# Kernel optimization log

Measured on AMD Instinct MI355X. Metric: run time of the kernel, lower is better.

## Reference

```python
import math
import jax, jax.numpy as jnp
import numpy as np
from jax import lax

D = 384; NHEAD = 12; NLAYERS = 4; H = 128; WIN = (128, 24); NS = (1, 10); B = 256; CONV_C = 128

def _interleave(s, c):
    # [s0,c0,s1,c1,...] along last dim (matches 0::2=sin, 1::2=cos)
    return jnp.stack([s, c], axis=-1).reshape(s.shape[:-1] + (s.shape[-1] * 2,))

def _pos_encoding():
    d3 = D // 3
    div = jnp.exp(jnp.arange(0, d3, 2, dtype=jnp.float32) * (-math.log(10000.0) / d3))
    coord = jnp.arange(H, dtype=jnp.float32) - H // 2
    pe1d = _interleave(jnp.sin(coord[:, None] * div), jnp.cos(coord[:, None] * div))  # (H, d3)
    pe_y = jnp.broadcast_to(pe1d[:, None, :], (H, H, d3))
    pe_x = jnp.broadcast_to(pe1d[None, :, :], (H, H, d3))
    ws = jnp.array(WIN, dtype=jnp.float32)
    pe_w = _interleave(jnp.sin(ws[:, None] * div), jnp.cos(ws[:, None] * div))  # (2, d3)
    pe_yx = jnp.concatenate([pe_y, pe_x], axis=-1)  # (H, H, 2*d3)
    pe = jnp.concatenate([
        jnp.broadcast_to(pe_yx[:, :, None, :], (H, H, len(WIN), 2 * d3)),
        jnp.broadcast_to(pe_w[None, None, :, :], (H, H, len(WIN), d3))], axis=-1)
    return pe  # (H, H, 2, D)

def _windows(img3, pos, ws):
    # img3: (B,3,H,W); pos: (n,2) int. Crop [y1:y2, x1:x2] then zero-pad bottom/right to ws x ws.
    hw = ws // 2
    y = jnp.clip(pos[:, 0], 0, H - 1); x = jnp.clip(pos[:, 1], 0, H - 1)
    y1 = jnp.maximum(0, y - hw); y2 = jnp.minimum(H, y + hw)
    x1 = jnp.maximum(0, x - hw); x2 = jnp.minimum(H, x + hw)
    r = jnp.arange(ws)
    rows = y1[:, None] + r; cols = x1[:, None] + r  # (n, ws)
    mask = (rows < y2[:, None])[:, :, None] & (cols < x2[:, None])[:, None, :]  # (n, ws, ws)
    win = img3[:, :, jnp.clip(rows, 0, H - 1)[:, :, None], jnp.clip(cols, 0, H - 1)[:, None, :]]  # (B,3,n,ws,ws)
    win = jnp.where(mask[None, None], win, 0.0)
    return jnp.transpose(win, (0, 2, 1, 3, 4))  # (B, n, 3, ws, ws)

def _layer_norm(x, g, b):
    m = x.mean(-1, keepdims=True)
    v = ((x - m) ** 2).mean(-1, keepdims=True)
    return (x - m) / jnp.sqrt(v + 1e-5) * g + b

def _encoder_layer(x, Wqkv, bqkv, Wo, bo, g1, b1, g2, b2, W1, bf1, W2, bf2):
    Bsz, S, _ = x.shape
    dh = D // NHEAD
    qkv = x @ Wqkv.T + bqkv
    q, k, v = jnp.split(qkv, 3, axis=-1)
    heads = lambda t: t.reshape(Bsz, S, NHEAD, dh).transpose(0, 2, 1, 3)
    q, k, v = heads(q), heads(k), heads(v)
    att = jax.nn.softmax(jnp.einsum('bhqd,bhkd->bhqk', q, k) / math.sqrt(dh), axis=-1)
    o = jnp.einsum('bhqk,bhkd->bhqd', att, v).transpose(0, 2, 1, 3).reshape(Bsz, S, D)
    x = _layer_norm(x + o @ Wo.T + bo, g1, b1)
    ff = jax.nn.relu(x @ W1.T + bf1) @ W2.T + bf2
    return _layer_norm(x + ff, g2, b2)

def _normalize(v):
    return v / jnp.maximum(jnp.linalg.norm(v, axis=1, keepdims=True), 1e-12)

def _forward(pos0, pos1, rgb_image, conv_w, conv_b, ext_w, ext_b, proj_w, proj_b,
             Wqkv, bqkv, Wo, bo, ln1g, ln1b, ln2g, ln2b, Wff1, bff1, Wff2, bff2,
             rw1, rb1, rw2, rb2, uw1, ub1, uw2, ub2):
    Bsz = rgb_image.shape[0]
    img3 = rgb_image[:, :3]
    win0 = _windows(img3, pos0, WIN[0]).reshape(Bsz * NS[0], 3, WIN[0], WIN[0])
    win1 = _windows(img3, pos1, WIN[1])  # (B, 10, 3, 24, 24)
    h = lax.conv_general_dilated(win0, conv_w, (4, 4), 'SAME')
    h = jax.nn.relu(h + conv_b[None, :, None, None])
    f0 = (h.mean((2, 3)) @ ext_w.T + ext_b).reshape(Bsz, NS[0], D)
    f1 = win1.reshape(Bsz, NS[1], -1) @ proj_w.T + proj_b  # (B,10,D)
    feats = jnp.concatenate([f0, f1], axis=1)  # (B, 11, D)
    pe = _pos_encoding()
    pp = jnp.concatenate([
        jnp.concatenate([pos0, jnp.zeros((NS[0], 1), pos0.dtype)], axis=1),
        jnp.concatenate([pos1, jnp.ones((NS[1], 1), pos1.dtype)], axis=1)], axis=0)  # (11, 3)
    pf = pe[pp[:, 0], pp[:, 1], pp[:, 2]]  # (11, D)
    x = feats + pf[None]
    for i in range(NLAYERS):
        x = _encoder_layer(x, Wqkv[i], bqkv[i], Wo[i], bo[i], ln1g[i], ln1b[i],
                           ln2g[i], ln2b[i], Wff1[i], bff1[i], Wff2[i], bff2[i])
    m = x.mean(axis=1)
    r = jax.nn.relu(m @ rw1.T + rb1) @ rw2.T + rb2
    r1, r2 = r[:, :3], r[:, 3:]
    r2 = r2 - jnp.sum(r1 * r2, axis=1, keepdims=True) * r1
    r3 = jnp.cross(r1, r2)
    R = jnp.concatenate([_normalize(r1), _normalize(r2), _normalize(r3)], axis=1)
    uv = jax.nn.sigmoid(jax.nn.relu(m @ uw1.T + ub1) @ uw2.T + ub2)
    return (uv, R)

def setup_inputs():
    key = jax.random.key(0)
    ks = iter(jax.random.split(key, 40))
    w = lambda *s: jax.random.normal(next(ks), s, jnp.float32) * 0.02
    return dict(
        rgb_image=jax.random.uniform(next(ks), (B, 4, H, H), jnp.float32),
        pos0=jax.random.randint(next(ks), (NS[0], 2), 0, H).astype(jnp.int32),
        pos1=jax.random.randint(next(ks), (NS[1], 2), 0, H).astype(jnp.int32),
        conv_w=w(CONV_C, 3, 7, 7), conv_b=jnp.zeros((CONV_C,), jnp.float32),
        ext_w=w(D, CONV_C), ext_b=jnp.zeros((D,), jnp.float32),
        proj_w=w(D, WIN[1] * WIN[1] * 3), proj_b=jnp.zeros((D,), jnp.float32),
        Wqkv=w(NLAYERS, 3 * D, D), bqkv=jnp.zeros((NLAYERS, 3 * D), jnp.float32),
        Wo=w(NLAYERS, D, D), bo=jnp.zeros((NLAYERS, D), jnp.float32),
        ln1g=jnp.ones((NLAYERS, D), jnp.float32), ln1b=jnp.zeros((NLAYERS, D), jnp.float32),
        ln2g=jnp.ones((NLAYERS, D), jnp.float32), ln2b=jnp.zeros((NLAYERS, D), jnp.float32),
        Wff1=w(NLAYERS, 2048, D), bff1=jnp.zeros((NLAYERS, 2048), jnp.float32),
        Wff2=w(NLAYERS, D, 2048), bff2=jnp.zeros((NLAYERS, D), jnp.float32),
        rw1=w(D, D), rb1=jnp.zeros((D,), jnp.float32),
        rw2=w(6, D), rb2=jnp.zeros((6,), jnp.float32),
        uw1=w(D, D), ub1=jnp.zeros((D,), jnp.float32),
        uw2=w(2, D), ub2=jnp.zeros((2,), jnp.float32),
    )

def reference(rgb_image, pos0, pos1, conv_w, conv_b, ext_w, ext_b, proj_w, proj_b,
              Wqkv, bqkv, Wo, bo, ln1g, ln1b, ln2g, ln2b, Wff1, bff1, Wff2, bff2,
              rw1, rb1, rw2, rb2, uw1, ub1, uw2, ub2):
    return _forward(pos0, pos1, rgb_image, conv_w, conv_b, ext_w, ext_b, proj_w, proj_b,
                    Wqkv, bqkv, Wo, bo, ln1g, ln1b, ln2g, ln2b, Wff1, bff1, Wff2, bff2,
                    rw1, rb1, rw2, rb2, uw1, ub1, uw2, ub2)
```

## Files before the change

kernel.cpp:

```cpp
#include <hip/hip_runtime.h>
#include <hip/hip_bf16.h>

#define B_ 256
#define S_ 11
#define D_ 384
#define NHEAD_ 12

typedef const float* bfp;
typedef __attribute__((ext_vector_type(8))) __bf16 bf16x8;
typedef __attribute__((ext_vector_type(4))) float f32x4;

__device__ __forceinline__ bf16x8 ld8_b64(const __bf16* p) {
    union { unsigned long long q[2]; bf16x8 v; } u;
    u.q[0] = *reinterpret_cast<const unsigned long long*>(p);
    u.q[1] = *reinterpret_cast<const unsigned long long*>(p + 4);
    return u.v;
}

__device__ __forceinline__ void gl16(const __bf16* g, __bf16* l) {
    __builtin_amdgcn_global_load_lds(
        (const __attribute__((address_space(1))) void*)g,
        (__attribute__((address_space(3))) void*)l, 16, 0, 0);
}

__global__ void f2b_k(const float* __restrict__ s, __bf16* __restrict__ d, int n4)
{
    int i = blockIdx.x * 256 + threadIdx.x;
    if (i >= n4) return;
    float4 v = reinterpret_cast<const float4*>(s)[i];
    union { __bf16 h[4]; unsigned long long u; } p;
    p.h[0] = (__bf16)v.x; p.h[1] = (__bf16)v.y;
    p.h[2] = (__bf16)v.z; p.h[3] = (__bf16)v.w;
    reinterpret_cast<unsigned long long*>(d)[i] = p.u;
}

__global__ void prep_wpad_k(bfp __restrict__ cw, __bf16* __restrict__ wpad)
{
    int e = blockIdx.x * 256 + threadIdx.x;
    if (e >= 3072) return;
    int r = e >> 5, g = e & 31;
    if (g >= 24) return;
    union { __bf16 h[8]; uint4 u; } w;
    #pragma unroll
    for (int kx = 0; kx < 8; ++kx) {
        float v = 0.f;
        if (g < 21 && kx < 7) v = cw[(size_t)r * 147 + g * 7 + kx];
        w.h[kx] = (__bf16)v;
    }
    *reinterpret_cast<uint4*>(&wpad[(size_t)r * 192 + g * 8]) = w.u;
}

__global__ __launch_bounds__(256) void gemm_bb_k(
    const __bf16* __restrict__ A, const __bf16* __restrict__ W,
    const float* __restrict__ bias, const float* __restrict__ resid,
    void* __restrict__ C_, int M, int N, int K, int mode, int outBf16, int kChunk)
{
    __shared__ __align__(16) __bf16 AsF[4096];
    __shared__ __align__(16) __bf16 WsF[4096];
    const int tid = threadIdx.x;
    const int bm = blockIdx.y * 64, bn = blockIdx.x * 64;
    const int z = blockIdx.z;
    int kStart = 0, kEnd = K;
    if (kChunk) { kStart = z * kChunk; kEnd = min(K, kStart + kChunk); }
    const int lane = tid & 63, wv = tid >> 6;
    const int wr = (wv >> 1) * 32, wc = (wv & 1) * 32;
    const int lr = lane & 15, lk = lane >> 4;
    const int c1 = tid + 256;
    const int r0 = tid >> 3, j0 = (tid & 7) ^ (r0 & 7);
    const int r1 = c1 >> 3,  j1 = (c1 & 7) ^ (r1 & 7);
    __bf16* ldsA0 = AsF + (wv << 9);
    __bf16* ldsA1 = AsF + 2048 + (wv << 9);
    __bf16* ldsW0 = WsF + (wv << 9);
    __bf16* ldsW1 = WsF + 2048 + (wv << 9);
    f32x4 acc[2][2] = {};
    for (int k0 = kStart; k0 < kEnd; k0 += 64) {
        const __bf16* ga0 = A + (size_t)(bm + r0) * K + k0 + j0 * 8;
        const __bf16* ga1 = A + (size_t)(bm + r1) * K + k0 + j1 * 8;
        const __bf16* gw0 = W + (size_t)(bn + r0) * K + k0 + j0 * 8;
        const __bf16* gw1 = W + (size_t)(bn + r1) * K + k0 + j1 * 8;
        __syncthreads();
        gl16(ga0, ldsA0);
        gl16(ga1, ldsA1);
        gl16(gw0, ldsW0);
        gl16(gw1, ldsW1);
        __syncthreads();
        #pragma unroll
        for (int s = 0; s < 2; ++s) {
            int j = s * 4 + lk;
            int ra0 = wr + lr,  ra1 = wr + 16 + lr;
            int rw0 = wc + lr,  rw1 = wc + 16 + lr;
            bf16x8 a0 = *reinterpret_cast<const bf16x8*>(&AsF[ra0 * 64 + ((j ^ (ra0 & 7)) << 3)]);
            bf16x8 a1 = *reinterpret_cast<const bf16x8*>(&AsF[ra1 * 64 + ((j ^ (ra1 & 7)) << 3)]);
            bf16x8 w0 = *reinterpret_cast<const bf16x8*>(&WsF[rw0 * 64 + ((j ^ (rw0 & 7)) << 3)]);
            bf16x8 w1 = *reinterpret_cast<const bf16x8*>(&WsF[rw1 * 64 + ((j ^ (rw1 & 7)) << 3)]);
            acc[0][0] = __builtin_amdgcn_mfma_f32_16x16x32_bf16(a0, w0, acc[0][0], 0, 0, 0);
            acc[0][1] = __builtin_amdgcn_mfma_f32_16x16x32_bf16(a0, w1, acc[0][1], 0, 0, 0);
            acc[1][0] = __builtin_amdgcn_mfma_f32_16x16x32_bf16(a1, w0, acc[1][0], 0, 0, 0);
            acc[1][1] = __builtin_amdgcn_mfma_f32_16x16x32_bf16(a1, w1, acc[1][1], 0, 0, 0);
        }
    }
    if (kChunk) {
        float* Cp = (float*)C_ + (size_t)z * M * N;
        #pragma unroll
        for (int m = 0; m < 2; ++m)
            #pragma unroll
            for (int n = 0; n < 2; ++n) {
                int col = bn + wc + n * 16 + lr;
                #pragma unroll
                for (int i = 0; i < 4; ++i) {
                    int row = bm + wr + m * 16 + lk * 4 + i;
                    Cp[(size_t)row * N + col] = acc[m][n][i];
                }
            }
    } else {
        #pragma unroll
        for (int m = 0; m < 2; ++m)
            #pragma unroll
            for (int n = 0; n < 2; ++n) {
                int col = bn + wc + n * 16 + lr;
                float bcol = bias[col];
                #pragma unroll
                for (int i = 0; i < 4; ++i) {
                    int row = bm + wr + m * 16 + lk * 4 + i;
                    float v = acc[m][n][i] + bcol;
                    if (mode == 1) v = fmaxf(v, 0.f);
                    if (mode == 2) v += resid[(size_t)row * N + col];
                    if (outBf16) ((__bf16*)C_)[(size_t)row * N + col] = (__bf16)v;
                    else         ((float*)C_)[(size_t)row * N + col] = v;
                }
            }
    }
}

__global__ __launch_bounds__(256) void convgemm_k(
    bfp __restrict__ img, const __bf16* __restrict__ wpad, bfp __restrict__ cb,
    const int* __restrict__ pos0, float* __restrict__ f0pre)
{
    __shared__ __align__(16) __bf16 Wlds[64][200];
    __shared__ __align__(16) __bf16 P[3][12][136];
    const int tid = threadIdx.x;
    const int blk = blockIdx.x;
    const int b = blk >> 3;
    const int bn = ((blk >> 2) & 1) * 64;
    const int mtg = blk & 3;
    int y = min(max(pos0[0], 0), 127), x = min(max(pos0[1], 0), 127);
    int y1 = max(0, y - 64), y2 = min(128, y + 64);
    int x1 = max(0, x - 64), x2 = min(128, x + 64);
    const int lane = tid & 63, wv = tid >> 6;
    const int wr = (wv >> 1) * 32, wc = (wv & 1) * 32;
    const int lr = lane & 15, lk = lane >> 4;
    const int oyl = wr >> 5;
    const int ox0 = lr, ox1 = 16 + lr;

    for (int e = tid; e < 1536; e += 256) {
        int r = e / 24, g = e - r * 24;
        uint4 q = *reinterpret_cast<const uint4*>(&wpad[(size_t)(bn + r) * 192 + g * 8]);
        *reinterpret_cast<uint4*>(&Wlds[r][g * 8]) = q;
    }

    float s0 = 0.f, s1 = 0.f;
    const float bc0 = cb[bn + wc + lr];
    const float bc1 = cb[bn + wc + 16 + lr];

    for (int t = 0; t < 4; ++t) {
        int mt = mtg * 4 + t;
        __syncthreads();
        for (int e = tid; e < 2448; e += 256) {
            int c = e / 816, rem = e - c * 816;
            int r2 = rem / 68, ip2 = (rem - r2 * 68) * 2;
            int rl = mt * 8 - 1 + r2;
            bool rok = (rl >= 0) && ((y1 + rl) < y2);
            const float* row = img + ((size_t)(b * 4 + c) * 128 + y1 + rl) * 128 + x1;
            int cl0 = ip2 - 1, cl1 = ip2;
            float v0 = 0.f, v1 = 0.f;
            if (rok && cl0 >= 0 && (x1 + cl0) < x2) v0 = row[cl0];
            if (rok && (x1 + cl1) < x2)             v1 = row[cl1];
            union { __bf16 h[2]; unsigned int u; } p;
            p.h[0] = (__bf16)v0; p.h[1] = (__bf16)v1;
            *reinterpret_cast<unsigned int*>(&P[c][r2][ip2]) = p.u;
        }
        __syncthreads();
        f32x4 acc[2][2] = {};
        #pragma unroll
        for (int kk = 0; kk < 6; ++kk) {
            int g = kk * 4 + lk;
            int c = g / 7, ky = g - c * 7;
            if (g >= 21) { c = 0; ky = 0; }
            const __bf16* prow = &P[c][oyl * 4 + ky][0];
            bf16x8 a0 = ld8_b64(prow + ox0 * 4);
            bf16x8 a1 = ld8_b64(prow + ox1 * 4);
            bf16x8 w0 = *reinterpret_cast<const bf16x8*>(&Wlds[wc + lr][g * 8]);
            bf16x8 w1 = *reinterpret_cast<const bf16x8*>(&Wlds[wc + 16 + lr][g * 8]);
            acc[0][0] = __builtin_amdgcn_mfma_f32_16x16x32_bf16(a0, w0, acc[0][0], 0, 0, 0);
            acc[0][1] = __builtin_amdgcn_mfma_f32_16x16x32_bf16(a0, w1, acc[0][1], 0, 0, 0);
            acc[1][0] = __builtin_amdgcn_mfma_f32_16x16x32_bf16(a1, w0, acc[1][0], 0, 0, 0);
            acc[1][1] = __builtin_amdgcn_mfma_f32_16x16x32_bf16(a1, w1, acc[1][1], 0, 0, 0);
        }
        #pragma unroll
        for (int m = 0; m < 2; ++m)
            #pragma unroll
            for (int i = 0; i < 4; ++i) {
                s0 += fmaxf(acc[m][0][i] + bc0, 0.f);
                s1 += fmaxf(acc[m][1][i] + bc1, 0.f);
            }
    }
    s0 += __shfl_xor(s0, 16); s0 += __shfl_xor(s0, 32);
    s1 += __shfl_xor(s1, 16); s1 += __shfl_xor(s1, 32);
    if (lk == 0) {
        atomicAdd(&f0pre[b * 128 + bn + wc + lr],      s0 * (1.f / 1024.f));
        atomicAdd(&f0pre[b * 128 + bn + wc + 16 + lr], s1 * (1.f / 1024.f));
    }
}

#define BM 64
#define BN 64
#define BK 16
__global__ __launch_bounds__(256) void gemm_k(
    const float* __restrict__ A, bfp __restrict__ W,
    bfp __restrict__ bias, const float* __restrict__ resid,
    float* __restrict__ C, int M, int N, int K, int mode)
{
    __shared__ __align__(16) float As[BK][BM + 4];
    __shared__ __align__(16) float Ws[BK][BN + 4];
    const int tx = threadIdx.x & 15, ty = threadIdx.x >> 4;
    const int bm = blockIdx.y * BM, bn = blockIdx.x * BN;
    float acc[4][4] = {};
    for (int k0 = 0; k0 < K; k0 += BK) {
        for (int e = threadIdx.x; e < BM * BK; e += 256) {
            int r = e >> 4, kk = e & 15;
            As[kk][r] = A[(size_t)(bm + r) * K + k0 + kk];
        }
        for (int e = threadIdx.x; e < BN * BK; e += 256) {
            int c = e >> 4, kk = e & 15;
            Ws[kk][c] = W[(size_t)(bn + c) * K + k0 + kk];
        }
        __syncthreads();
        #pragma unroll
        for (int kk = 0; kk < BK; ++kk) {
            float4 av = *reinterpret_cast<const float4*>(&As[kk][ty * 4]);
            float4 wv = *reinterpret_cast<const float4*>(&Ws[kk][tx * 4]);
            float a[4] = {av.x, av.y, av.z, av.w};
            float w[4] = {wv.x, wv.y, wv.z, wv.w};
            #pragma unroll
            for (int i = 0; i < 4; ++i)
                #pragma unroll
                for (int j = 0; j < 4; ++j) acc[i][j] += a[i] * w[j];
        }
        __syncthreads();
    }
    #pragma unroll
    for (int i = 0; i < 4; ++i) {
        int row = bm + ty * 4 + i;
        #pragma unroll
        for (int j = 0; j < 4; ++j) {
            int col = bn + tx * 4 + j;
            float v = acc[i][j] + bias[col];
            if (mode == 1) v = fmaxf(v, 0.f);
            if (mode == 2) v += resid[(size_t)row * N + col];
            C[(size_t)row * N + col] = v;
        }
    }
}

__global__ void f0_k(const float* __restrict__ f0pre, bfp __restrict__ ew,
                     bfp __restrict__ eb, float* __restrict__ fbuf0)
{
    int b = blockIdx.x, d = threadIdx.x;
    __shared__ float pre[128];
    if (d < 128) pre[d] = f0pre[b * 128 + d];
    __syncthreads();
    float acc = eb[d];
    for (int co = 0; co < 128; ++co) acc += pre[co] * ew[d * 128 + co];
    fbuf0[b * 384 + d] = acc;
}

__global__ void win1_k(bfp __restrict__ img, const int* __restrict__ pos1,
                       __bf16* __restrict__ w1)
{
    int i = blockIdx.x * 256 + threadIdx.x;
    if (i >= B_ * 10 * 1728) return;
    int cc = i % 24, r = (i / 24) % 24, c = (i / 576) % 3, s = (i / 1728) % 10, b = i / 17280;
    int y = min(max(pos1[s * 2], 0), 127), x = min(max(pos1[s * 2 + 1], 0), 127);
    int y1 = max(0, y - 12), y2 = min(128, y + 12);
    int x1 = max(0, x - 12), x2 = min(128, x + 12);
    float v = 0.f;
    if ((y1 + r) < y2 && (x1 + cc) < x2)
        v = img[((size_t)(b * 4 + c) * 128 + (y1 + r)) * 128 + (x1 + cc)];
    w1[i] = (__bf16)v;
}

__global__ void pf_k(const int* __restrict__ pos0, const int* __restrict__ pos1,
                     float* __restrict__ pf)
{
    int d = threadIdx.x;
    const float c1 = -logf(10000.f) / 128.f;
    for (int s = 0; s < 11; ++s) {
        int py, px, pw;
        if (s == 0) { py = pos0[0]; px = pos0[1]; pw = 0; }
        else { py = pos1[(s - 1) * 2]; px = pos1[(s - 1) * 2 + 1]; pw = 1; }
        float coordv; int dd = d;
        if (d < 128) coordv = (float)(py - 64);
        else if (d < 256) { coordv = (float)(px - 64); dd = d - 128; }
        else { coordv = (pw == 0) ? 128.f : 24.f; dd = d - 256; }
        int i = dd >> 1;
        float div = expf((float)(2 * i) * c1);
        float ang = coordv * div;
        pf[s * 384 + d] = (dd & 1) ? cosf(ang) : sinf(ang);
    }
}

__global__ void assemble_k(const float* __restrict__ f0, const float* __restrict__ f1,
                           const float* __restrict__ pf, float* __restrict__ x,
                           __bf16* __restrict__ xb)
{
    int i = blockIdx.x * 256 + threadIdx.x;
    if (i >= B_ * S_ * D_) return;
    int d = i % 384, s = (i / 384) % 11, b = i / (384 * 11);
    float f = (s == 0) ? f0[b * 384 + d] : f1[((size_t)(b * 10) + (s - 1)) * 384 + d];
    float v = f + pf[s * 384 + d];
    x[i] = v;
    xb[i] = (__bf16)v;
}

__global__ __launch_bounds__(128) void attn_k(const float* __restrict__ qkv,
                                              __bf16* __restrict__ obuf)
{
    int b = blockIdx.x / NHEAD_, h = blockIdx.x % NHEAD_;
    __shared__ float q[11][32], k[11][32], v[11][32], att[11][12];
    for (int e = threadIdx.x; e < 352; e += 128) {
        int s = e >> 5, d = e & 31;
        size_t base = (size_t)(b * 11 + s) * 1152 + h * 32 + d;
        q[s][d] = qkv[base];
        k[s][d] = qkv[base + 384];
        v[s][d] = qkv[base + 768];
    }
    __syncthreads();
    if (threadIdx.x < 121) {
        int i = threadIdx.x / 11, j = threadIdx.x % 11;
        float s = 0.f;
        #pragma unroll
        for (int d = 0; d < 32; ++d) s += q[i][d] * k[j][d];
        att[i][j] = s * 0.17677669529663687f;
    }
    __syncthreads();
    if (threadIdx.x < 11) {
        int i = threadIdx.x;
        float mx = att[i][0];
        for (int j = 1; j < 11; ++j) mx = fmaxf(mx, att[i][j]);
        float e_[11], sum = 0.f;
        for (int j = 0; j < 11; ++j) { e_[j] = expf(att[i][j] - mx); sum += e_[j]; }
        float inv = 1.f / sum;
        for (int j = 0; j < 11; ++j) att[i][j] = e_[j] * inv;
    }
    __syncthreads();
    for (int e = threadIdx.x; e < 352; e += 128) {
        int i = e >> 5, d = e & 31;
        float s = 0.f;
        #pragma unroll
        for (int j = 0; j < 11; ++j) s += att[i][j] * v[j][d];
        obuf[(size_t)(b * 11 + i) * 384 + h * 32 + d] = (__bf16)s;
    }
}

__global__ __launch_bounds__(512) void ln_k(const float* __restrict__ parts, int nparts,
                                            const float* __restrict__ resid,
                                            const float* __restrict__ bias,
                                            bfp g, bfp be, float* __restrict__ xo,
                                            __bf16* __restrict__ xb)
{
    int row = blockIdx.x * 8 + (threadIdx.x >> 6);
    int lane = threadIdx.x & 63;
    const size_t MN = (size_t)2816 * 384;
    float v[6];
    float s = 0.f, sq = 0.f;
    #pragma unroll
    for (int j = 0; j < 6; ++j) {
        int d = lane + 64 * j;
        size_t off = (size_t)row * 384 + d;
        float t = resid[off] + bias[d];
        for (int z = 0; z < nparts; ++z) t += parts[z * MN + off];
        v[j] = t; s += t; sq += t * t;
    }
    #pragma unroll
    for (int o = 32; o >= 1; o >>= 1) { s += __shfl_xor(s, o); sq += __shfl_xor(sq, o); }
    float mean = s * (1.f / 384.f);
    float var = sq * (1.f / 384.f) - mean * mean;
    float inv = rsqrtf(var + 1e-5f);
    float* xr = xo + (size_t)row * 384;
    __bf16* xbr = xb + (size_t)row * 384;
    #pragma unroll
    for (int j = 0; j < 6; ++j) {
        int d = lane + 64 * j;
        float o = (v[j] - mean) * inv * g[d] + be[d];
        xr[d] = o;
        xbr[d] = (__bf16)o;
    }
}

__global__ void mean_k(const float* __restrict__ x, float* __restrict__ m)
{
    int b = blockIdx.x, d = threadIdx.x;
    float s = 0.f;
    for (int si = 0; si < 11; ++si) s += x[((size_t)b * 11 + si) * 384 + d];
    m[b * 384 + d] = s * (1.f / 11.f);
}

__global__ __launch_bounds__(64) void head_k(const float* __restrict__ h1,
    const float* __restrict__ h2, bfp __restrict__ rw2, bfp __restrict__ rb2,
    bfp __restrict__ uw2, bfp __restrict__ ub2, float* __restrict__ out)
{
    int b = blockIdx.x, lane = threadIdx.x;
    float acc[8] = {};
    for (int d = lane; d < 384; d += 64) {
        float a1 = h1[b * 384 + d], a2 = h2[b * 384 + d];
        #pragma unroll
        for (int o = 0; o < 6; ++o) acc[o] += a1 * rw2[o * 384 + d];
        acc[6] += a2 * uw2[d];
        acc[7] += a2 * uw2[384 + d];
    }
    #pragma unroll
    for (int o = 0; o < 8; ++o)
        #pragma unroll
        for (int off = 32; off >= 1; off >>= 1) acc[o] += __shfl_xor(acc[o], off);
    if (lane == 0) {
        float r[6];
        for (int o = 0; o < 6; ++o) r[o] = acc[o] + rb2[o];
        float u0 = acc[6] + ub2[0], u1 = acc[7] + ub2[1];
        float dot12 = r[0] * r[3] + r[1] * r[4] + r[2] * r[5];
        float q2x = r[3] - dot12 * r[0], q2y = r[4] - dot12 * r[1], q2z = r[5] - dot12 * r[2];
        float q3x = r[1] * q2z - r[2] * q2y;
        float q3y = r[2] * q2x - r[0] * q2z;
        float q3z = r[0] * q2y - r[1] * q2x;
        float n1 = fmaxf(sqrtf(r[0]*r[0] + r[1]*r[1] + r[2]*r[2]), 1e-12f);
        float n2 = fmaxf(sqrtf(q2x*q2x + q2y*q2y + q2z*q2z), 1e-12f);
        float n3 = fmaxf(sqrtf(q3x*q3x + q3y*q3y + q3z*q3z), 1e-12f);
        out[b * 2 + 0] = 1.f / (1.f + expf(-u0));
        out[b * 2 + 1] = 1.f / (1.f + expf(-u1));
        float* R = out + B_ * 2 + b * 9;
        R[0] = r[0] / n1; R[1] = r[1] / n1; R[2] = r[2] / n1;
        R[3] = q2x / n2;  R[4] = q2y / n2;  R[5] = q2z / n2;
        R[6] = q3x / n3;  R[7] = q3y / n3;  R[8] = q3z / n3;
    }
}

extern "C" void kernel_launch(void* const* d_in, const int* in_sizes, int n_in,
                              void* d_out, int out_size, void* d_ws, size_t ws_size,
                              hipStream_t stream)
{
    bfp rgb     = (bfp)d_in[0];
    const int* pos0 = (const int*)d_in[1];
    const int* pos1 = (const int*)d_in[2];
    bfp conv_w  = (bfp)d_in[3];
    bfp conv_b  = (bfp)d_in[4];
    bfp ext_w   = (bfp)d_in[5];
    bfp ext_b   = (bfp)d_in[6];
    bfp proj_w  = (bfp)d_in[7];
    bfp proj_b  = (bfp)d_in[8];
    bfp Wqkv    = (bfp)d_in[9];
    bfp bqkv    = (bfp)d_in[10];
    bfp Wo      = (bfp)d_in[11];
    bfp bo      = (bfp)d_in[12];
    bfp ln1g    = (bfp)d_in[13];
    bfp ln1b    = (bfp)d_in[14];
    bfp ln2g    = (bfp)d_in[15];
    bfp ln2b    = (bfp)d_in[16];
    bfp Wff1    = (bfp)d_in[17];
    bfp bff1    = (bfp)d_in[18];
    bfp Wff2    = (bfp)d_in[19];
    bfp bff2    = (bfp)d_in[20];
    bfp rw1     = (bfp)d_in[21];
    bfp rb1     = (bfp)d_in[22];
    bfp rw2     = (bfp)d_in[23];
    bfp rb2     = (bfp)d_in[24];
    bfp uw1     = (bfp)d_in[25];
    bfp ub1     = (bfp)d_in[26];
    bfp uw2     = (bfp)d_in[27];
    bfp ub2     = (bfp)d_in[28];

    float* ws = (float*)d_ws;
    float*  X      = ws;
    float*  Y      = ws + 1081344;
    float*  QKV    = ws + 2162688;
    float*  FBUF1  = QKV;
    float*  FBUF0  = QKV + 983040;
    float*  F0PRE  = QKV + 983040 + 98304;
    __bf16* OBUFb  = (__bf16*)(ws + 5406720);
    float*  H1     = ws + 5947392;
    float*  H2     = ws + 6045696;
    __bf16* FFH16  = (__bf16*)(ws + 6144000);
    __bf16* WIN1F16= FFH16;
    float*  PF     = ws + 9027584;
    float*  M_     = ws + 9031808;
    __bf16* Xb     = (__bf16*)(ws + 9130112);
    __bf16* projWb = (__bf16*)(ws + 9670784);
    __bf16* WqkvB  = (__bf16*)(ws + 10002560);
    __bf16* WoB    = (__bf16*)(ws + 10887296);
    __bf16* Wff1B  = (__bf16*)(ws + 11182208);
    __bf16* Wff2B  = (__bf16*)(ws + 12755072);
    __bf16* WpadC  = (__bf16*)(ws + 14327936);

    hipMemsetAsync(F0PRE, 0, 256 * 128 * sizeof(float), stream);

    f2b_k<<<648,  256, 0, stream>>>(proj_w, projWb, 165888);
    f2b_k<<<1728, 256, 0, stream>>>(Wqkv,   WqkvB,  442368);
    f2b_k<<<576,  256, 0, stream>>>(Wo,     WoB,    147456);
    f2b_k<<<3072, 256, 0, stream>>>(Wff1,   Wff1B,  786432);
    f2b_k<<<3072, 256, 0, stream>>>(Wff2,   Wff2B,  786432);
    prep_wpad_k<<<16, 256, 0, stream>>>(conv_w, WpadC);

    convgemm_k<<<2048, 256, 0, stream>>>(rgb, WpadC, conv_b, pos0, F0PRE);
    win1_k<<<(B_ * 10 * 1728 + 255) / 256, 256, 0, stream>>>(rgb, pos1, WIN1F16);
    f0_k<<<256, 384, 0, stream>>>(F0PRE, ext_w, ext_b, FBUF0);
    gemm_bb_k<<<dim3(6, 40), 256, 0, stream>>>(WIN1F16, projWb, proj_b, nullptr,
                                               FBUF1, 2560, 384, 1728, 0, 0, 0);
    pf_k<<<1, 384, 0, stream>>>(pos0, pos1, PF);
    assemble_k<<<(B_ * S_ * D_ + 255) / 256, 256, 0, stream>>>(FBUF0, FBUF1, PF, X, Xb);

    for (int i = 0; i < 4; ++i) {
        gemm_bb_k<<<dim3(18, 44), 256, 0, stream>>>(
            Xb, WqkvB + (size_t)i * 1152 * 384, bqkv + i * 1152, nullptr, QKV,
            2816, 1152, 384, 0, 0, 0);
        attn_k<<<B_ * NHEAD_, 128, 0, stream>>>(QKV, OBUFb);
        gemm_bb_k<<<dim3(6, 44, 2), 256, 0, stream>>>(
            OBUFb, WoB + (size_t)i * 384 * 384, nullptr, nullptr, QKV,
            2816, 384, 384, 0, 0, 192);
        ln_k<<<352, 512, 0, stream>>>(QKV, 2, X, bo + i * 384,
                                      ln1g + i * 384, ln1b + i * 384, X, Xb);
        gemm_bb_k<<<dim3(32, 44), 256, 0, stream>>>(
            Xb, Wff1B + (size_t)i * 2048 * 384, bff1 + i * 2048, nullptr, FFH16,
            2816, 2048, 384, 1, 1, 0);
        gemm_bb_k<<<dim3(6, 44, 3), 256, 0, stream>>>(
            FFH16, Wff2B + (size_t)i * 384 * 2048, nullptr, nullptr, QKV,
            2816, 384, 2048, 0, 0, 704);
        ln_k<<<352, 512, 0, stream>>>(QKV, 3, X, bff2 + i * 384,
                                      ln2g + i * 384, ln2b + i * 384, X, Xb);
    }

    mean_k<<<256, 384, 0, stream>>>(X, M_);
    gemm_k<<<dim3(384 / BN, 256 / BM), 256, 0, stream>>>(M_, rw1, rb1, nullptr, H1, 256, 384, 384, 1);
    gemm_k<<<dim3(384 / BN, 256 / BM), 256, 0, stream>>>(M_, uw1, ub1, nullptr, H2, 256, 384, 384, 1);
    head_k<<<256, 64, 0, stream>>>(H1, H2, rw2, rb2, uw2, ub2, (float*)d_out);
}
```

Measured before the change: 523.7 us.

## Double-buffer GEMM LDS loads, merge prep kernels, split-K the projection GEMM

Converts the bf16 GEMM main loop to a two-stage LDS double buffer, so the async global-to-LDS loads for the next K tile are issued before the MFMAs on the current tile, and one barrier per step replaces two. Merges the five weight-conversion launches, the conv weight padding and the positional-feature kernel into one prep kernel to cut launch overhead. Splits the window projection GEMM into two K chunks for more blocks, with bias and the partial-sum reduction folded into the assemble kernel. LDS use per block doubles, which may lower occupancy.

```diff
diff --git a/kernel.cpp b/kernel.cpp
--- a/kernel.cpp
+++ b/kernel.cpp
@@ -23,31 +23,61 @@
         (__attribute__((address_space(3))) void*)l, 16, 0, 0);
 }
 
-__global__ void f2b_k(const float* __restrict__ s, __bf16* __restrict__ d, int n4)
+__global__ void prep_k(const float* __restrict__ proj_w, const float* __restrict__ Wqkv,
+                       const float* __restrict__ Wo, const float* __restrict__ Wff1,
+                       const float* __restrict__ Wff2,
+                       __bf16* __restrict__ projWb, __bf16* __restrict__ WqkvB,
+                       __bf16* __restrict__ WoB, __bf16* __restrict__ Wff1B,
+                       __bf16* __restrict__ Wff2B,
+                       const float* __restrict__ cw, __bf16* __restrict__ wpad,
+                       const int* __restrict__ pos0, const int* __restrict__ pos1,
+                       float* __restrict__ pf)
 {
     int i = blockIdx.x * 256 + threadIdx.x;
-    if (i >= n4) return;
-    float4 v = reinterpret_cast<const float4*>(s)[i];
+    const float* s; __bf16* d; int off;
+    if      (i < 165888)  { s = proj_w; d = projWb; off = i; }
+    else if (i < 608256)  { s = Wqkv;   d = WqkvB;  off = i - 165888; }
+    else if (i < 755712)  { s = Wo;     d = WoB;    off = i - 608256; }
+    else if (i < 1542144) { s = Wff1;   d = Wff1B;  off = i - 755712; }
+    else if (i < 2328576) { s = Wff2;   d = Wff2B;  off = i - 1542144; }
+    else if (i < 2331648) {
+        int e = i - 2328576;
+        int r = e >> 5, g = e & 31;
+        if (g >= 24) return;
+        union { __bf16 h[8]; uint4 u; } w;
+        #pragma unroll
+        for (int kx = 0; kx < 8; ++kx) {
+            float v = 0.f;
+            if (g < 21 && kx < 7) v = cw[(size_t)r * 147 + g * 7 + kx];
+            w.h[kx] = (__bf16)v;
+        }
+        *reinterpret_cast<uint4*>(&wpad[(size_t)r * 192 + g * 8]) = w.u;
+        return;
+    }
+    else if (i < 2332032) {
+        int dd0 = i - 2331648;
+        const float c1 = -logf(10000.f) / 128.f;
+        for (int ss = 0; ss < 11; ++ss) {
+            int py, px, pw;
+            if (ss == 0) { py = pos0[0]; px = pos0[1]; pw = 0; }
+            else { py = pos1[(ss - 1) * 2]; px = pos1[(ss - 1) * 2 + 1]; pw = 1; }
+            float coordv; int dd = dd0;
+            if (dd0 < 128) coordv = (float)(py - 64);
+            else if (dd0 < 256) { coordv = (float)(px - 64); dd = dd0 - 128; }
+            else { coordv = (pw == 0) ? 128.f : 24.f; dd = dd0 - 256; }
+            int ii = dd >> 1;
+            float div = expf((float)(2 * ii) * c1);
+            float ang = coordv * div;
+            pf[ss * 384 + dd0] = (dd & 1) ? cosf(ang) : sinf(ang);
+        }
+        return;
+    }
+    else return;
+    float4 v = reinterpret_cast<const float4*>(s)[off];
     union { __bf16 h[4]; unsigned long long u; } p;
     p.h[0] = (__bf16)v.x; p.h[1] = (__bf16)v.y;
     p.h[2] = (__bf16)v.z; p.h[3] = (__bf16)v.w;
-    reinterpret_cast<unsigned long long*>(d)[i] = p.u;
-}
-
-__global__ void prep_wpad_k(bfp __restrict__ cw, __bf16* __restrict__ wpad)
-{
-    int e = blockIdx.x * 256 + threadIdx.x;
-    if (e >= 3072) return;
-    int r = e >> 5, g = e & 31;
-    if (g >= 24) return;
-    union { __bf16 h[8]; uint4 u; } w;
-    #pragma unroll
-    for (int kx = 0; kx < 8; ++kx) {
-        float v = 0.f;
-        if (g < 21 && kx < 7) v = cw[(size_t)r * 147 + g * 7 + kx];
-        w.h[kx] = (__bf16)v;
-    }
-    *reinterpret_cast<uint4*>(&wpad[(size_t)r * 192 + g * 8]) = w.u;
+    reinterpret_cast<unsigned long long*>(d)[off] = p.u;
 }
 
 __global__ __launch_bounds__(256) void gemm_bb_k(
@@ -55,8 +85,8 @@
     const float* __restrict__ bias, const float* __restrict__ resid,
     void* __restrict__ C_, int M, int N, int K, int mode, int outBf16, int kChunk)
 {
-    __shared__ __align__(16) __bf16 AsF[4096];
-    __shared__ __align__(16) __bf16 WsF[4096];
+    __shared__ __align__(16) __bf16 AsF[2][4096];
+    __shared__ __align__(16) __bf16 WsF[2][4096];
     const int tid = threadIdx.x;
     const int bm = blockIdx.y * 64, bn = blockIdx.x * 64;
     const int z = blockIdx.z;
@@ -68,37 +98,44 @@
     const int c1 = tid + 256;
     const int r0 = tid >> 3, j0 = (tid & 7) ^ (r0 & 7);
     const int r1 = c1 >> 3,  j1 = (c1 & 7) ^ (r1 & 7);
-    __bf16* ldsA0 = AsF + (wv << 9);
-    __bf16* ldsA1 = AsF + 2048 + (wv << 9);
-    __bf16* ldsW0 = WsF + (wv << 9);
-    __bf16* ldsW1 = WsF + 2048 + (wv << 9);
+    const size_t gaoff0 = (size_t)(bm + r0) * K + j0 * 8;
+    const size_t gaoff1 = (size_t)(bm + r1) * K + j1 * 8;
+    const size_t gwoff0 = (size_t)(bn + r0) * K + j0 * 8;
+    const size_t gwoff1 = (size_t)(bn + r1) * K + j1 * 8;
     f32x4 acc[2][2] = {};
+
+#define STAGE_(bf, kk) do {                                   \
+        gl16(A + gaoff0 + (kk), &AsF[bf][(wv << 9)]);         \
+        gl16(A + gaoff1 + (kk), &AsF[bf][2048 + (wv << 9)]);  \
+        gl16(W + gwoff0 + (kk), &WsF[bf][(wv << 9)]);         \
+        gl16(W + gwoff1 + (kk), &WsF[bf][2048 + (wv << 9)]);  \
+    } while (0)
+
+    STAGE_(0, kStart);
+    __syncthreads();
+    int cur = 0;
     for (int k0 = kStart; k0 < kEnd; k0 += 64) {
-        const __bf16* ga0 = A + (size_t)(bm + r0) * K + k0 + j0 * 8;
-        const __bf16* ga1 = A + (size_t)(bm + r1) * K + k0 + j1 * 8;
-        const __bf16* gw0 = W + (size_t)(bn + r0) * K + k0 + j0 * 8;
-        const __bf16* gw1 = W + (size_t)(bn + r1) * K + k0 + j1 * 8;
-        __syncthreads();
-        gl16(ga0, ldsA0);
-        gl16(ga1, ldsA1);
-        gl16(gw0, ldsW0);
-        gl16(gw1, ldsW1);
-        __syncthreads();
+        if (k0 + 64 < kEnd) STAGE_(cur ^ 1, k0 + 64);
+        const __bf16* Ab = AsF[cur];
+        const __bf16* Wb = WsF[cur];
         #pragma unroll
         for (int s = 0; s < 2; ++s) {
             int j = s * 4 + lk;
             int ra0 = wr + lr,  ra1 = wr + 16 + lr;
             int rw0 = wc + lr,  rw1 = wc + 16 + lr;
-            bf16x8 a0 = *reinterpret_cast<const bf16x8*>(&AsF[ra0 * 64 + ((j ^ (ra0 & 7)) << 3)]);
-            bf16x8 a1 = *reinterpret_cast<const bf16x8*>(&AsF[ra1 * 64 + ((j ^ (ra1 & 7)) << 3)]);
-            bf16x8 w0 = *reinterpret_cast<const bf16x8*>(&WsF[rw0 * 64 + ((j ^ (rw0 & 7)) << 3)]);
-            bf16x8 w1 = *reinterpret_cast<const bf16x8*>(&WsF[rw1 * 64 + ((j ^ (rw1 & 7)) << 3)]);
+            bf16x8 a0 = *reinterpret_cast<const bf16x8*>(&Ab[ra0 * 64 + ((j ^ (ra0 & 7)) << 3)]);
+            bf16x8 a1 = *reinterpret_cast<const bf16x8*>(&Ab[ra1 * 64 + ((j ^ (ra1 & 7)) << 3)]);
+            bf16x8 w0 = *reinterpret_cast<const bf16x8*>(&Wb[rw0 * 64 + ((j ^ (rw0 & 7)) << 3)]);
+            bf16x8 w1 = *reinterpret_cast<const bf16x8*>(&Wb[rw1 * 64 + ((j ^ (rw1 & 7)) << 3)]);
             acc[0][0] = __builtin_amdgcn_mfma_f32_16x16x32_bf16(a0, w0, acc[0][0], 0, 0, 0);
             acc[0][1] = __builtin_amdgcn_mfma_f32_16x16x32_bf16(a0, w1, acc[0][1], 0, 0, 0);
             acc[1][0] = __builtin_amdgcn_mfma_f32_16x16x32_bf16(a1, w0, acc[1][0], 0, 0, 0);
             acc[1][1] = __builtin_amdgcn_mfma_f32_16x16x32_bf16(a1, w1, acc[1][1], 0, 0, 0);
         }
-    }
+        __syncthreads();
+        cur ^= 1;
+    }
+#undef STAGE_
     if (kChunk) {
         float* Cp = (float*)C_ + (size_t)z * M * N;
         #pragma unroll
@@ -289,34 +326,20 @@
     w1[i] = (__bf16)v;
 }
 
-__global__ void pf_k(const int* __restrict__ pos0, const int* __restrict__ pos1,
-                     float* __restrict__ pf)
-{
-    int d = threadIdx.x;
-    const float c1 = -logf(10000.f) / 128.f;
-    for (int s = 0; s < 11; ++s) {
-        int py, px, pw;
-        if (s == 0) { py = pos0[0]; px = pos0[1]; pw = 0; }
-        else { py = pos1[(s - 1) * 2]; px = pos1[(s - 1) * 2 + 1]; pw = 1; }
-        float coordv; int dd = d;
-        if (d < 128) coordv = (float)(py - 64);
-        else if (d < 256) { coordv = (float)(px - 64); dd = d - 128; }
-        else { coordv = (pw == 0) ? 128.f : 24.f; dd = d - 256; }
-        int i = dd >> 1;
-        float div = expf((float)(2 * i) * c1);
-        float ang = coordv * div;
-        pf[s * 384 + d] = (dd & 1) ? cosf(ang) : sinf(ang);
-    }
-}
-
-__global__ void assemble_k(const float* __restrict__ f0, const float* __restrict__ f1,
+__global__ void assemble_k(const float* __restrict__ f0, const float* __restrict__ p0,
+                           const float* __restrict__ p1, const float* __restrict__ projb,
                            const float* __restrict__ pf, float* __restrict__ x,
                            __bf16* __restrict__ xb)
 {
     int i = blockIdx.x * 256 + threadIdx.x;
     if (i >= B_ * S_ * D_) return;
     int d = i % 384, s = (i / 384) % 11, b = i / (384 * 11);
-    float f = (s == 0) ? f0[b * 384 + d] : f1[((size_t)(b * 10) + (s - 1)) * 384 + d];
+    float f;
+    if (s == 0) f = f0[b * 384 + d];
+    else {
+        size_t o = ((size_t)(b * 10) + (s - 1)) * 384 + d;
+        f = p0[o] + p1[o] + projb[d];
+    }
     float v = f + pf[s * 384 + d];
     x[i] = v;
     xb[i] = (__bf16)v;
@@ -479,11 +502,11 @@
 
     float* ws = (float*)d_ws;
     float*  X      = ws;
-    float*  Y      = ws + 1081344;
     float*  QKV    = ws + 2162688;
-    float*  FBUF1  = QKV;
     float*  FBUF0  = QKV + 983040;
     float*  F0PRE  = QKV + 983040 + 98304;
+    float*  PP0    = QKV + 1114112;
+    float*  PP1    = QKV + 1114112 + 983040;
     __bf16* OBUFb  = (__bf16*)(ws + 5406720);
     float*  H1     = ws + 5947392;
     float*  H2     = ws + 6045696;
@@ -501,20 +524,17 @@
 
     hipMemsetAsync(F0PRE, 0, 256 * 128 * sizeof(float), stream);
 
-    f2b_k<<<648,  256, 0, stream>>>(proj_w, projWb, 165888);
-    f2b_k<<<1728, 256, 0, stream>>>(Wqkv,   WqkvB,  442368);
-    f2b_k<<<576,  256, 0, stream>>>(Wo,     WoB,    147456);
-    f2b_k<<<3072, 256, 0, stream>>>(Wff1,   Wff1B,  786432);
-    f2b_k<<<3072, 256, 0, stream>>>(Wff2,   Wff2B,  786432);
-    prep_wpad_k<<<16, 256, 0, stream>>>(conv_w, WpadC);
+    prep_k<<<9110, 256, 0, stream>>>(proj_w, Wqkv, Wo, Wff1, Wff2,
+                                     projWb, WqkvB, WoB, Wff1B, Wff2B,
+                                     conv_w, WpadC, pos0, pos1, PF);
 
     convgemm_k<<<2048, 256, 0, stream>>>(rgb, WpadC, conv_b, pos0, F0PRE);
     win1_k<<<(B_ * 10 * 1728 + 255) / 256, 256, 0, stream>>>(rgb, pos1, WIN1F16);
     f0_k<<<256, 384, 0, stream>>>(F0PRE, ext_w, ext_b, FBUF0);
-    gemm_bb_k<<<dim3(6, 40), 256, 0, stream>>>(WIN1F16, projWb, proj_b, nullptr,
-                                               FBUF1, 2560, 384, 1728, 0, 0, 0);
-    pf_k<<<1, 384, 0, stream>>>(pos0, pos1, PF);
-    assemble_k<<<(B_ * S_ * D_ + 255) / 256, 256, 0, stream>>>(FBUF0, FBUF1, PF, X, Xb);
+    gemm_bb_k<<<dim3(6, 40, 2), 256, 0, stream>>>(WIN1F16, projWb, nullptr, nullptr,
+                                                  PP0, 2560, 384, 1728, 0, 0, 896);
+    assemble_k<<<(B_ * S_ * D_ + 255) / 256, 256, 0, stream>>>(FBUF0, PP0, PP1, proj_b,
+                                                               PF, X, Xb);
 
     for (int i = 0; i < 4; ++i) {
         gemm_bb_k<<<dim3(18, 44), 256, 0, stream>>>(
```

After: 520.5 us. About the same (-0.6%).
